# Kernel optimization log

Hardware: AMD Instinct MI355X
Metric: run time of the kernel (lower is better)

## Reference

```python
import jax, jax.numpy as jnp
import numpy as np

GAMMA1 = 4.0

def setup_inputs() -> dict:
    key = jax.random.key(0)
    k1, k2 = jax.random.split(key)
    image_feature = jax.random.normal(k1, (128, 17, 17, 1024), dtype=jnp.float32)
    word_vector = jax.random.normal(k2, (128, 32, 1024), dtype=jnp.float32)
    return {"image_feature": image_feature, "word_vector": word_vector}

def reference(image_feature, word_vector):
    B, H, W, D = image_feature.shape
    T = word_vector.shape[1]
    # context: [B, HW, D]
    context = image_feature.reshape(B, H * W, D)
    # attn scores: [B, HW, T] = context @ word_vector^T
    attn = jnp.einsum('bnd,btd->bnt', context, word_vector)
    # first softmax over words (last dim of [B*HW, T])
    attn = jax.nn.softmax(attn, axis=-1)
    # transpose to [B, T, HW], scale by gamma1, softmax over regions
    attn = jnp.transpose(attn, (0, 2, 1))
    attn = jax.nn.softmax(GAMMA1 * attn, axis=-1)
    # region_context: [B, D, T] = context^T @ attn^T
    region_context = jnp.einsum('bnd,btn->bdt', context, attn)
    return region_context
```

## Files before the change

### kernel.cpp

```cpp
#include <hip/hip_runtime.h>

#define B_ 128
#define N_ 289
#define D_ 1024
#define T_ 32
#define GAMMA1 4.0f

__global__ __launch_bounds__(256) void damsm_attn_a(
    const float* __restrict__ img, const float* __restrict__ word,
    float* __restrict__ E)
{
    __shared__ float s_ctx[64][68];
    __shared__ float s_word[32][68];

    const int b   = blockIdx.y;
    const int n0  = blockIdx.x * 64;
    const int tid = threadIdx.x;
    const int i   = tid >> 4;
    const int j   = tid & 15;

    const float* __restrict__ imgb  = img  + (size_t)(b * N_) * D_;
    const float* __restrict__ wordb = word + (size_t)(b * T_) * D_;

    float acc[4][2];
#pragma unroll
    for (int k = 0; k < 4; ++k) { acc[k][0] = 0.f; acc[k][1] = 0.f; }

    for (int d0 = 0; d0 < D_; d0 += 64) {
#pragma unroll
        for (int k = 0; k < 4; ++k) {
            int idx = tid + 256 * k;
            int nl  = idx >> 4;
            int dq  = idx & 15;
            float4 v = make_float4(0.f, 0.f, 0.f, 0.f);
            int n = n0 + nl;
            if (n < N_)
                v = *(const float4*)(imgb + (size_t)n * D_ + d0 + dq * 4);
            *(float4*)(&s_ctx[nl][dq * 4]) = v;
        }
#pragma unroll
        for (int k = 0; k < 2; ++k) {
            int idx = tid + 256 * k;
            int tl  = idx >> 4;
            int dq  = idx & 15;
            float4 v = *(const float4*)(wordb + (size_t)tl * D_ + d0 + dq * 4);
            *(float4*)(&s_word[tl][dq * 4]) = v;
        }
        __syncthreads();

#pragma unroll
        for (int d4 = 0; d4 < 16; ++d4) {
            float4 w0 = *(const float4*)(&s_word[j][d4 * 4]);
            float4 w1 = *(const float4*)(&s_word[j + 16][d4 * 4]);
#pragma unroll
            for (int k = 0; k < 4; ++k) {
                float4 c = *(const float4*)(&s_ctx[i * 4 + k][d4 * 4]);
                acc[k][0] = fmaf(c.x, w0.x, fmaf(c.y, w0.y,
                            fmaf(c.z, w0.z, fmaf(c.w, w0.w, acc[k][0]))));
                acc[k][1] = fmaf(c.x, w1.x, fmaf(c.y, w1.y,
                            fmaf(c.z, w1.z, fmaf(c.w, w1.w, acc[k][1]))));
            }
        }
        __syncthreads();
    }

#pragma unroll
    for (int k = 0; k < 4; ++k) {
        float m = fmaxf(acc[k][0], acc[k][1]);
#pragma unroll
        for (int s = 1; s < 16; s <<= 1) m = fmaxf(m, __shfl_xor(m, s));
        float e0 = __expf(acc[k][0] - m);
        float e1 = __expf(acc[k][1] - m);
        float ssum = e0 + e1;
#pragma unroll
        for (int s = 1; s < 16; s <<= 1) ssum += __shfl_xor(ssum, s);
        float inv = 1.0f / ssum;
        float E0 = __expf(GAMMA1 * (e0 * inv));
        float E1 = __expf(GAMMA1 * (e1 * inv));
        int n = n0 + i * 4 + k;
        if (n < N_) {
            float* dst = E + (size_t)(b * N_ + n) * T_;
            dst[j]      = E0;
            dst[j + 16] = E1;
        }
    }
}

__global__ __launch_bounds__(256) void damsm_attn_b(
    const float* __restrict__ img, const float* __restrict__ E,
    float* __restrict__ out)
{
    __shared__ float s_E[N_][T_];
    __shared__ float s_red[32][32];
    __shared__ float s_csinv[T_];
    __shared__ float s_ctx[32][128];

    const int b   = blockIdx.y;
    const int d0  = blockIdx.x * 128;
    const int tid = threadIdx.x;
    const int p   = tid >> 3;
    const int q   = tid & 7;

    const float* __restrict__ Eb   = E   + (size_t)b * N_ * T_;
    const float* __restrict__ imgb = img + (size_t)(b * N_) * D_;

    for (int idx = tid; idx < (N_ * T_) / 4; idx += 256)
        ((float4*)s_E)[idx] = ((const float4*)Eb)[idx];
    __syncthreads();

    {
        float4 part = make_float4(0.f, 0.f, 0.f, 0.f);
        for (int n = p; n < N_; n += 32) {
            float4 e = *(const float4*)(&s_E[n][q * 4]);
            part.x += e.x; part.y += e.y; part.z += e.z; part.w += e.w;
        }
        *(float4*)(&s_red[p][q * 4]) = part;
    }
    __syncthreads();
    if (tid < T_) {
        float s = 0.f;
        for (int pp = 0; pp < 32; ++pp) s += s_red[pp][tid];
        s_csinv[tid] = 1.0f / s;
    }
    __syncthreads();

    float acc[4][4];
#pragma unroll
    for (int a = 0; a < 4; ++a)
#pragma unroll
        for (int c = 0; c < 4; ++c) acc[a][c] = 0.f;

    for (int nc = 0; nc < 288; nc += 32) {
#pragma unroll
        for (int k = 0; k < 4; ++k) {
            int idx = tid + 256 * k;
            int nl  = idx >> 5;
            int dq  = idx & 31;
            *(float4*)(&s_ctx[nl][dq * 4]) =
                *(const float4*)(imgb + (size_t)(nc + nl) * D_ + d0 + dq * 4);
        }
        __syncthreads();
#pragma unroll 4
        for (int nn = 0; nn < 32; ++nn) {
            float4 c = *(const float4*)(&s_ctx[nn][p * 4]);
            float4 e = *(const float4*)(&s_E[nc + nn][q * 4]);
            acc[0][0] = fmaf(c.x, e.x, acc[0][0]);
            acc[0][1] = fmaf(c.x, e.y, acc[0][1]);
            acc[0][2] = fmaf(c.x, e.z, acc[0][2]);
            acc[0][3] = fmaf(c.x, e.w, acc[0][3]);
            acc[1][0] = fmaf(c.y, e.x, acc[1][0]);
            acc[1][1] = fmaf(c.y, e.y, acc[1][1]);
            acc[1][2] = fmaf(c.y, e.z, acc[1][2]);
            acc[1][3] = fmaf(c.y, e.w, acc[1][3]);
            acc[2][0] = fmaf(c.z, e.x, acc[2][0]);
            acc[2][1] = fmaf(c.z, e.y, acc[2][1]);
            acc[2][2] = fmaf(c.z, e.z, acc[2][2]);
            acc[2][3] = fmaf(c.z, e.w, acc[2][3]);
            acc[3][0] = fmaf(c.w, e.x, acc[3][0]);
            acc[3][1] = fmaf(c.w, e.y, acc[3][1]);
            acc[3][2] = fmaf(c.w, e.z, acc[3][2]);
            acc[3][3] = fmaf(c.w, e.w, acc[3][3]);
        }
        __syncthreads();
    }
    {
        float4 e = *(const float4*)(&s_E[288][q * 4]);
        float4 c = *(const float4*)(imgb + (size_t)288 * D_ + d0 + p * 4);
        acc[0][0] = fmaf(c.x, e.x, acc[0][0]);
        acc[0][1] = fmaf(c.x, e.y, acc[0][1]);
        acc[0][2] = fmaf(c.x, e.z, acc[0][2]);
        acc[0][3] = fmaf(c.x, e.w, acc[0][3]);
        acc[1][0] = fmaf(c.y, e.x, acc[1][0]);
        acc[1][1] = fmaf(c.y, e.y, acc[1][1]);
        acc[1][2] = fmaf(c.y, e.z, acc[1][2]);
        acc[1][3] = fmaf(c.y, e.w, acc[1][3]);
        acc[2][0] = fmaf(c.z, e.x, acc[2][0]);
        acc[2][1] = fmaf(c.z, e.y, acc[2][1]);
        acc[2][2] = fmaf(c.z, e.z, acc[2][2]);
        acc[2][3] = fmaf(c.z, e.w, acc[2][3]);
        acc[3][0] = fmaf(c.w, e.x, acc[3][0]);
        acc[3][1] = fmaf(c.w, e.y, acc[3][1]);
        acc[3][2] = fmaf(c.w, e.z, acc[3][2]);
        acc[3][3] = fmaf(c.w, e.w, acc[3][3]);
    }

    float4 ci = *(const float4*)(&s_csinv[q * 4]);
#pragma unroll
    for (int di = 0; di < 4; ++di) {
        int d = d0 + p * 4 + di;
        float4 v;
        v.x = acc[di][0] * ci.x;
        v.y = acc[di][1] * ci.y;
        v.z = acc[di][2] * ci.z;
        v.w = acc[di][3] * ci.w;
        *(float4*)(out + (size_t)(b * D_ + d) * T_ + q * 4) = v;
    }
}

extern "C" void kernel_launch(void* const* d_in, const int* in_sizes, int n_in,
                              void* d_out, int out_size, void* d_ws, size_t ws_size,
                              hipStream_t stream) {
    const float* img  = (const float*)d_in[0];
    const float* word = (const float*)d_in[1];
    float* out = (float*)d_out;
    float* E   = (float*)d_ws;

    dim3 blk(256);
    dim3 grdA(5, 128);
    hipLaunchKernelGGL(damsm_attn_a, grdA, blk, 0, stream, img, word, E);
    dim3 grdB(8, 128);
    hipLaunchKernelGGL(damsm_attn_b, grdB, blk, 0, stream, img, E, out);
}
```

Before: 303.7 us.

## Use split-bf16 MFMA for both attention GEMMs with XCD-aware block mapping

Both matmul stages now run on MFMA 16x16x32 bf16 instructions instead of scalar FMAs. Each fp32 value is split into a bf16 hi/lo pair, and three MFMAs per tile (hi*hi, hi*lo, lo*hi) recover near-fp32 accuracy. Kernel A uses 32-row tiles with 128 threads and remaps blocks so each XCD handles contiguous batches for better L2 reuse. Kernel B transposes E and the context into packed shared memory, computes column sums with shared atomics, and stages output through shared memory for coalesced stores. The costs are the split/pack conversion work, the extra MFMA passes, and slightly lower precision than true fp32.

Result: slower. 335.6 us (+10.5%).

```diff
diff --git a/kernel.cpp b/kernel.cpp
--- a/kernel.cpp
+++ b/kernel.cpp
@@ -1,87 +1,128 @@
 #include <hip/hip_runtime.h>
 
-#define B_ 128
-#define N_ 289
-#define D_ 1024
-#define T_ 32
+#define NB 128
+#define NN 289
+#define ND 1024
+#define NT 32
 #define GAMMA1 4.0f
 
-__global__ __launch_bounds__(256) void damsm_attn_a(
+typedef __attribute__((ext_vector_type(4))) float f32x4;
+typedef __attribute__((ext_vector_type(8))) short bf8;
+
+__device__ inline void split2(float x, ushort &h, ushort &l) {
+    uint u = __float_as_uint(x);
+    h = (ushort)(u >> 16);
+    float hf = __uint_as_float(u & 0xFFFF0000u);
+    l = (ushort)(__float_as_uint(x - hf) >> 16);
+}
+__device__ inline uint packhl(float x) {
+    uint u = __float_as_uint(x);
+    float hf = __uint_as_float(u & 0xFFFF0000u);
+    uint lo = __float_as_uint(x - hf) >> 16;
+    return (u & 0xFFFF0000u) | lo;
+}
+__device__ inline void unpack8(const uint *u, bf8 &hi, bf8 &lo) {
+    union { uint w[4]; bf8 v; } H, L;
+#pragma unroll
+    for (int k = 0; k < 4; ++k) {
+        H.w[k] = (u[2 * k] >> 16) | (u[2 * k + 1] & 0xFFFF0000u);
+        L.w[k] = (u[2 * k] & 0xFFFFu) | (u[2 * k + 1] << 16);
+    }
+    hi = H.v; lo = L.v;
+}
+
+__global__ __launch_bounds__(128) void damsm_attn_a(
     const float* __restrict__ img, const float* __restrict__ word,
     float* __restrict__ E)
 {
-    __shared__ float s_ctx[64][68];
-    __shared__ float s_word[32][68];
-
-    const int b   = blockIdx.y;
-    const int n0  = blockIdx.x * 64;
+    __shared__ ushort sAh[32][72], sAl[32][72];
+    __shared__ ushort sBh[32][72], sBl[32][72];
+
+    const int bid = blockIdx.x;
+    const int xcd = bid & 7;
+    const int s   = bid >> 3;
+    const int b   = xcd * 16 + s / 10;
+    const int m   = s % 10;
+    const int n0  = m * 32;
+
     const int tid = threadIdx.x;
-    const int i   = tid >> 4;
-    const int j   = tid & 15;
-
-    const float* __restrict__ imgb  = img  + (size_t)(b * N_) * D_;
-    const float* __restrict__ wordb = word + (size_t)(b * T_) * D_;
-
-    float acc[4][2];
-#pragma unroll
-    for (int k = 0; k < 4; ++k) { acc[k][0] = 0.f; acc[k][1] = 0.f; }
-
-    for (int d0 = 0; d0 < D_; d0 += 64) {
-#pragma unroll
-        for (int k = 0; k < 4; ++k) {
-            int idx = tid + 256 * k;
-            int nl  = idx >> 4;
-            int dq  = idx & 15;
+    const int w   = tid >> 6;
+    const int l   = tid & 63;
+    const int lr  = l & 15;
+    const int lh  = l >> 4;
+
+    const float* __restrict__ imgb  = img  + (size_t)b * NN * ND;
+    const float* __restrict__ wordb = word + (size_t)b * NT * ND;
+
+    f32x4 acc[2];
+#pragma unroll
+    for (int ct = 0; ct < 2; ++ct) acc[ct] = (f32x4){0.f, 0.f, 0.f, 0.f};
+
+    for (int kc = 0; kc < 16; ++kc) {
+#pragma unroll
+        for (int it = 0; it < 4; ++it) {
+            int idx = tid + 128 * it;
+            int row = idx >> 4;
+            int q   = idx & 15;
+            int n   = n0 + row;
             float4 v = make_float4(0.f, 0.f, 0.f, 0.f);
-            int n = n0 + nl;
-            if (n < N_)
-                v = *(const float4*)(imgb + (size_t)n * D_ + d0 + dq * 4);
-            *(float4*)(&s_ctx[nl][dq * 4]) = v;
-        }
-#pragma unroll
-        for (int k = 0; k < 2; ++k) {
-            int idx = tid + 256 * k;
-            int tl  = idx >> 4;
-            int dq  = idx & 15;
-            float4 v = *(const float4*)(wordb + (size_t)tl * D_ + d0 + dq * 4);
-            *(float4*)(&s_word[tl][dq * 4]) = v;
-        }
-        __syncthreads();
-
-#pragma unroll
-        for (int d4 = 0; d4 < 16; ++d4) {
-            float4 w0 = *(const float4*)(&s_word[j][d4 * 4]);
-            float4 w1 = *(const float4*)(&s_word[j + 16][d4 * 4]);
-#pragma unroll
-            for (int k = 0; k < 4; ++k) {
-                float4 c = *(const float4*)(&s_ctx[i * 4 + k][d4 * 4]);
-                acc[k][0] = fmaf(c.x, w0.x, fmaf(c.y, w0.y,
-                            fmaf(c.z, w0.z, fmaf(c.w, w0.w, acc[k][0]))));
-                acc[k][1] = fmaf(c.x, w1.x, fmaf(c.y, w1.y,
-                            fmaf(c.z, w1.z, fmaf(c.w, w1.w, acc[k][1]))));
+            if (n < NN)
+                v = *(const float4*)(imgb + (size_t)n * ND + kc * 64 + q * 4);
+            union { ushort us[4]; uint2 u2; } H, L;
+            split2(v.x, H.us[0], L.us[0]); split2(v.y, H.us[1], L.us[1]);
+            split2(v.z, H.us[2], L.us[2]); split2(v.w, H.us[3], L.us[3]);
+            *(uint2*)(&sAh[row][q * 4]) = H.u2;
+            *(uint2*)(&sAl[row][q * 4]) = L.u2;
+        }
+#pragma unroll
+        for (int it = 0; it < 4; ++it) {
+            int idx = tid + 128 * it;
+            int row = idx >> 4;
+            int q   = idx & 15;
+            float4 v = *(const float4*)(wordb + (size_t)row * ND + kc * 64 + q * 4);
+            union { ushort us[4]; uint2 u2; } H, L;
+            split2(v.x, H.us[0], L.us[0]); split2(v.y, H.us[1], L.us[1]);
+            split2(v.z, H.us[2], L.us[2]); split2(v.w, H.us[3], L.us[3]);
+            *(uint2*)(&sBh[row][q * 4]) = H.u2;
+            *(uint2*)(&sBl[row][q * 4]) = L.u2;
+        }
+        __syncthreads();
+
+#pragma unroll
+        for (int ks = 0; ks < 2; ++ks) {
+            const int ko = ks * 32 + 8 * lh;
+            bf8 ah = *(const bf8*)(&sAh[16 * w + lr][ko]);
+            bf8 al = *(const bf8*)(&sAl[16 * w + lr][ko]);
+#pragma unroll
+            for (int ct = 0; ct < 2; ++ct) {
+                bf8 bh = *(const bf8*)(&sBh[16 * ct + lr][ko]);
+                bf8 bl = *(const bf8*)(&sBl[16 * ct + lr][ko]);
+                acc[ct] = __builtin_amdgcn_mfma_f32_16x16x32_bf16(ah, bh, acc[ct], 0, 0, 0);
+                acc[ct] = __builtin_amdgcn_mfma_f32_16x16x32_bf16(ah, bl, acc[ct], 0, 0, 0);
+                acc[ct] = __builtin_amdgcn_mfma_f32_16x16x32_bf16(al, bh, acc[ct], 0, 0, 0);
             }
         }
         __syncthreads();
     }
 
 #pragma unroll
-    for (int k = 0; k < 4; ++k) {
-        float m = fmaxf(acc[k][0], acc[k][1]);
-#pragma unroll
-        for (int s = 1; s < 16; s <<= 1) m = fmaxf(m, __shfl_xor(m, s));
-        float e0 = __expf(acc[k][0] - m);
-        float e1 = __expf(acc[k][1] - m);
-        float ssum = e0 + e1;
-#pragma unroll
-        for (int s = 1; s < 16; s <<= 1) ssum += __shfl_xor(ssum, s);
-        float inv = 1.0f / ssum;
+    for (int r = 0; r < 4; ++r) {
+        float v0 = acc[0][r], v1 = acc[1][r];
+        float mx = fmaxf(v0, v1);
+#pragma unroll
+        for (int sh = 1; sh < 16; sh <<= 1) mx = fmaxf(mx, __shfl_xor(mx, sh));
+        float e0 = __expf(v0 - mx), e1 = __expf(v1 - mx);
+        float ss = e0 + e1;
+#pragma unroll
+        for (int sh = 1; sh < 16; sh <<= 1) ss += __shfl_xor(ss, sh);
+        float inv = 1.0f / ss;
         float E0 = __expf(GAMMA1 * (e0 * inv));
         float E1 = __expf(GAMMA1 * (e1 * inv));
-        int n = n0 + i * 4 + k;
-        if (n < N_) {
-            float* dst = E + (size_t)(b * N_ + n) * T_;
-            dst[j]      = E0;
-            dst[j + 16] = E1;
+        int n = n0 + 16 * w + 4 * lh + r;
+        if (n < NN) {
+            float* dst = E + ((size_t)b * NN + n) * NT;
+            dst[lr]      = E0;
+            dst[lr + 16] = E1;
         }
     }
 }
@@ -90,110 +131,121 @@
     const float* __restrict__ img, const float* __restrict__ E,
     float* __restrict__ out)
 {
-    __shared__ float s_E[N_][T_];
-    __shared__ float s_red[32][32];
-    __shared__ float s_csinv[T_];
-    __shared__ float s_ctx[32][128];
-
-    const int b   = blockIdx.y;
-    const int d0  = blockIdx.x * 128;
+    __shared__ uint  sEt[32 * 321];
+    __shared__ uint  sCt[128 * 33];
+    __shared__ float sOut[128 * 36];
+    __shared__ float sCs[NT];
+
+    const int bid = blockIdx.x;
+    const int b   = bid >> 3;
+    const int d0  = (bid & 7) * 128;
+
     const int tid = threadIdx.x;
-    const int p   = tid >> 3;
-    const int q   = tid & 7;
-
-    const float* __restrict__ Eb   = E   + (size_t)b * N_ * T_;
-    const float* __restrict__ imgb = img + (size_t)(b * N_) * D_;
-
-    for (int idx = tid; idx < (N_ * T_) / 4; idx += 256)
-        ((float4*)s_E)[idx] = ((const float4*)Eb)[idx];
-    __syncthreads();
-
-    {
-        float4 part = make_float4(0.f, 0.f, 0.f, 0.f);
-        for (int n = p; n < N_; n += 32) {
-            float4 e = *(const float4*)(&s_E[n][q * 4]);
-            part.x += e.x; part.y += e.y; part.z += e.z; part.w += e.w;
-        }
-        *(float4*)(&s_red[p][q * 4]) = part;
-    }
-    __syncthreads();
-    if (tid < T_) {
-        float s = 0.f;
-        for (int pp = 0; pp < 32; ++pp) s += s_red[pp][tid];
-        s_csinv[tid] = 1.0f / s;
-    }
-    __syncthreads();
-
-    float acc[4][4];
-#pragma unroll
-    for (int a = 0; a < 4; ++a)
-#pragma unroll
-        for (int c = 0; c < 4; ++c) acc[a][c] = 0.f;
-
-    for (int nc = 0; nc < 288; nc += 32) {
-#pragma unroll
-        for (int k = 0; k < 4; ++k) {
-            int idx = tid + 256 * k;
-            int nl  = idx >> 5;
-            int dq  = idx & 31;
-            *(float4*)(&s_ctx[nl][dq * 4]) =
-                *(const float4*)(imgb + (size_t)(nc + nl) * D_ + d0 + dq * 4);
-        }
-        __syncthreads();
-#pragma unroll 4
-        for (int nn = 0; nn < 32; ++nn) {
-            float4 c = *(const float4*)(&s_ctx[nn][p * 4]);
-            float4 e = *(const float4*)(&s_E[nc + nn][q * 4]);
-            acc[0][0] = fmaf(c.x, e.x, acc[0][0]);
-            acc[0][1] = fmaf(c.x, e.y, acc[0][1]);
-            acc[0][2] = fmaf(c.x, e.z, acc[0][2]);
-            acc[0][3] = fmaf(c.x, e.w, acc[0][3]);
-            acc[1][0] = fmaf(c.y, e.x, acc[1][0]);
-            acc[1][1] = fmaf(c.y, e.y, acc[1][1]);
-            acc[1][2] = fmaf(c.y, e.z, acc[1][2]);
-            acc[1][3] = fmaf(c.y, e.w, acc[1][3]);
-            acc[2][0] = fmaf(c.z, e.x, acc[2][0]);
-            acc[2][1] = fmaf(c.z, e.y, acc[2][1]);
-            acc[2][2] = fmaf(c.z, e.z, acc[2][2]);
-            acc[2][3] = fmaf(c.z, e.w, acc[2][3]);
-            acc[3][0] = fmaf(c.w, e.x, acc[3][0]);
-            acc[3][1] = fmaf(c.w, e.y, acc[3][1]);
-            acc[3][2] = fmaf(c.w, e.z, acc[3][2]);
-            acc[3][3] = fmaf(c.w, e.w, acc[3][3]);
-        }
-        __syncthreads();
-    }
-    {
-        float4 e = *(const float4*)(&s_E[288][q * 4]);
-        float4 c = *(const float4*)(imgb + (size_t)288 * D_ + d0 + p * 4);
-        acc[0][0] = fmaf(c.x, e.x, acc[0][0]);
-        acc[0][1] = fmaf(c.x, e.y, acc[0][1]);
-        acc[0][2] = fmaf(c.x, e.z, acc[0][2]);
-        acc[0][3] = fmaf(c.x, e.w, acc[0][3]);
-        acc[1][0] = fmaf(c.y, e.x, acc[1][0]);
-        acc[1][1] = fmaf(c.y, e.y, acc[1][1]);
-        acc[1][2] = fmaf(c.y, e.z, acc[1][2]);
-        acc[1][3] = fmaf(c.y, e.w, acc[1][3]);
-        acc[2][0] = fmaf(c.z, e.x, acc[2][0]);
-        acc[2][1] = fmaf(c.z, e.y, acc[2][1]);
-        acc[2][2] = fmaf(c.z, e.z, acc[2][2]);
-        acc[2][3] = fmaf(c.z, e.w, acc[2][3]);
-        acc[3][0] = fmaf(c.w, e.x, acc[3][0]);
-        acc[3][1] = fmaf(c.w, e.y, acc[3][1]);
-        acc[3][2] = fmaf(c.w, e.z, acc[3][2]);
-        acc[3][3] = fmaf(c.w, e.w, acc[3][3]);
-    }
-
-    float4 ci = *(const float4*)(&s_csinv[q * 4]);
-#pragma unroll
-    for (int di = 0; di < 4; ++di) {
-        int d = d0 + p * 4 + di;
-        float4 v;
-        v.x = acc[di][0] * ci.x;
-        v.y = acc[di][1] * ci.y;
-        v.z = acc[di][2] * ci.z;
-        v.w = acc[di][3] * ci.w;
-        *(float4*)(out + (size_t)(b * D_ + d) * T_ + q * 4) = v;
+    const int w   = tid >> 6;
+    const int l   = tid & 63;
+    const int lr  = l & 15;
+    const int lh  = l >> 4;
+
+    const float* __restrict__ Eb   = E   + (size_t)b * NN * NT;
+    const float* __restrict__ imgb = img + (size_t)b * NN * ND;
+
+    if (tid < NT) sCs[tid] = 0.f;
+    __syncthreads();
+
+    for (int idx = tid; idx < (NN * NT) / 4; idx += 256) {
+        int n  = idx >> 3;
+        int tq = idx & 7;
+        float4 v = *(const float4*)(Eb + (size_t)idx * 4);
+        sEt[(tq * 4 + 0) * 321 + n] = packhl(v.x);
+        sEt[(tq * 4 + 1) * 321 + n] = packhl(v.y);
+        sEt[(tq * 4 + 2) * 321 + n] = packhl(v.z);
+        sEt[(tq * 4 + 3) * 321 + n] = packhl(v.w);
+        atomicAdd(&sCs[tq * 4 + 0], v.x);
+        atomicAdd(&sCs[tq * 4 + 1], v.y);
+        atomicAdd(&sCs[tq * 4 + 2], v.z);
+        atomicAdd(&sCs[tq * 4 + 3], v.w);
+    }
+    for (int idx = tid; idx < 32 * 32; idx += 256) {
+        int t = idx >> 5;
+        int n = NN + (idx & 31);
+        sEt[t * 321 + n] = 0u;
+    }
+    __syncthreads();
+    if (tid < NT) sCs[tid] = 1.0f / sCs[tid];
+    __syncthreads();
+
+    f32x4 acc[2][2];
+#pragma unroll
+    for (int rt = 0; rt < 2; ++rt)
+#pragma unroll
+        for (int ct = 0; ct < 2; ++ct) acc[rt][ct] = (f32x4){0.f, 0.f, 0.f, 0.f};
+
+    for (int kc = 0; kc < 10; ++kc) {
+        const int nc0 = kc * 32;
+#pragma unroll
+        for (int it = 0; it < 4; ++it) {
+            int idx = tid + 256 * it;
+            int nn  = idx >> 5;
+            int q   = idx & 31;
+            int n   = nc0 + nn;
+            float4 v = make_float4(0.f, 0.f, 0.f, 0.f);
+            if (n < NN)
+                v = *(const float4*)(imgb + (size_t)n * ND + d0 + q * 4);
+            sCt[(q * 4 + 0) * 33 + nn] = packhl(v.x);
+            sCt[(q * 4 + 1) * 33 + nn] = packhl(v.y);
+            sCt[(q * 4 + 2) * 33 + nn] = packhl(v.z);
+            sCt[(q * 4 + 3) * 33 + nn] = packhl(v.w);
+        }
+        __syncthreads();
+
+        uint ua[8];
+        bf8 ahi[2], alo[2];
+#pragma unroll
+        for (int rt = 0; rt < 2; ++rt) {
+            int base = (16 * rt + lr) * 321 + nc0 + 8 * lh;
+#pragma unroll
+            for (int e = 0; e < 8; ++e) ua[e] = sEt[base + e];
+            unpack8(ua, ahi[rt], alo[rt]);
+        }
+#pragma unroll
+        for (int ct = 0; ct < 2; ++ct) {
+            int base = (32 * w + 16 * ct + lr) * 33 + 8 * lh;
+            uint ub[8];
+#pragma unroll
+            for (int e = 0; e < 8; ++e) ub[e] = sCt[base + e];
+            bf8 bhi, blo;
+            unpack8(ub, bhi, blo);
+#pragma unroll
+            for (int rt = 0; rt < 2; ++rt) {
+                acc[rt][ct] = __builtin_amdgcn_mfma_f32_16x16x32_bf16(ahi[rt], bhi, acc[rt][ct], 0, 0, 0);
+                acc[rt][ct] = __builtin_amdgcn_mfma_f32_16x16x32_bf16(ahi[rt], blo, acc[rt][ct], 0, 0, 0);
+                acc[rt][ct] = __builtin_amdgcn_mfma_f32_16x16x32_bf16(alo[rt], bhi, acc[rt][ct], 0, 0, 0);
+            }
+        }
+        __syncthreads();
+    }
+
+#pragma unroll
+    for (int rt = 0; rt < 2; ++rt)
+#pragma unroll
+        for (int ct = 0; ct < 2; ++ct) {
+            int dl = 32 * w + 16 * ct + lr;
+#pragma unroll
+            for (int r = 0; r < 4; ++r) {
+                int t = 16 * rt + 4 * lh + r;
+                sOut[dl * 36 + t] = acc[rt][ct][r] * sCs[t];
+            }
+        }
+    __syncthreads();
+
+    float* __restrict__ outb = out + (size_t)b * ND * NT;
+#pragma unroll
+    for (int it = 0; it < 4; ++it) {
+        int idx = tid + 256 * it;
+        int dl  = idx >> 3;
+        int tq  = idx & 7;
+        float4 v = *(const float4*)(&sOut[dl * 36 + tq * 4]);
+        *(float4*)(outb + (size_t)(d0 + dl) * NT + tq * 4) = v;
     }
 }
 
@@ -205,9 +257,6 @@
     float* out = (float*)d_out;
     float* E   = (float*)d_ws;
 
-    dim3 blk(256);
-    dim3 grdA(5, 128);
-    hipLaunchKernelGGL(damsm_attn_a, grdA, blk, 0, stream, img, word, E);
-    dim3 grdB(8, 128);
-    hipLaunchKernelGGL(damsm_attn_b, grdB, blk, 0, stream, img, E, out);
-}
+    hipLaunchKernelGGL(damsm_attn_a, dim3(1280), dim3(128), 0, stream, img, word, E);
+    hipLaunchKernelGGL(damsm_attn_b, dim3(1024), dim3(256), 0, stream, img, E, out);
+}
```
